# Optimization experiments

Measured on AMD Instinct MI355X. Metric: run time of the kernel, lower is better.

## Reference

```python
import jax, jax.numpy as jnp
import numpy as np

B = 128
NE = 14951   # num entities (FB15k)
NR = 1345    # num relations
D = 200      # complex embedding dim (real+imag concatenated)
NL = 116     # number of numerical literal relations


def setup_inputs() -> dict:
    key = jax.random.key(0)
    ks = jax.random.split(key, 8)
    e1_idx = jax.random.randint(ks[0], (B,), 0, NE)
    r_idx = jax.random.randint(ks[1], (B,), 0, NR)
    E = jax.random.normal(ks[2], (NE, D), dtype=jnp.float32) * 0.1
    R = jax.random.normal(ks[3], (NR, D), dtype=jnp.float32) * 0.1
    nf_weights = jax.random.normal(ks[4], (NR, NL), dtype=jnp.float32) * 0.1
    numerical_literals = jax.random.uniform(ks[5], (NE, NL), dtype=jnp.float32)
    c = jax.random.normal(ks[6], (NL,), dtype=jnp.float32) * 0.1
    var = jax.random.uniform(ks[7], (NL,), dtype=jnp.float32) * 0.5 + 0.1  # positive variances
    return {"e1_idx": e1_idx, "r_idx": r_idx, "E": E, "R": R,
            "nf_weights": nf_weights, "numerical_literals": numerical_literals,
            "c": c, "var": var}


def reference(e1_idx, r_idx, E, R, nf_weights, numerical_literals, c, var):
    d2 = E.shape[1] // 2
    e1 = E[e1_idx]            # [B, D]
    r = R[r_idx]              # [B, D]
    e1_real, e1_img = e1[:, :d2], e1[:, d2:]
    r_real, r_img = r[:, :d2], r[:, d2:]
    E_real, E_img = E[:, :d2], E[:, d2:]

    # ComplEx score against all entities: [B, NE]
    score_l = ((e1_real * r_real) @ E_real.T
               + (e1_real * r_img) @ E_img.T
               + (e1_img * r_real) @ E_img.T
               - (e1_img * r_img) @ E_real.T)

    # KBLN numerical-literal branch
    n_h = numerical_literals[e1_idx]                         # [B, NL]
    n = n_h[:, None, :] - numerical_literals[None, :, :]     # [B, NE, NL]
    phi = jnp.exp(-jnp.square(n - c) / var)                  # RBF, [B, NE, NL]
    w_nf = nf_weights[r_idx]                                 # [B, NL]
    score_n = jnp.einsum('ben,bn->be', phi, w_nf)            # [B, NE]

    return jax.nn.sigmoid(score_l + score_n)
```

## Files before the change

### kernel.cpp

```cpp
#include <hip/hip_runtime.h>

#define B     128
#define NE    14951
#define NEP   14976
#define NR    1345
#define D     200
#define NL    116
#define D2    100
#define EB    4
#define LOG2E 1.4426950408889634f

#define OFF_ET8  0
#define OFF_LT4  (OFF_ET8 + 25*NEP*4)
#define OFF_WB   (OFF_LT4 + 29*NEP*2)
#define OFF_UB   (OFF_WB + 128*200)
#define OFF_FB   (OFF_UB + 128*116)
#define OFF_NQ   (OFF_FB + 128*116)
#define WS_FLOATS (OFF_NQ + 128)
#define WS_NEEDED ((size_t)WS_FLOATS * 4)

__device__ __forceinline__ unsigned bf16rne(float f) {
    unsigned u = __float_as_uint(f);
    u += 0x7FFFu + ((u >> 16) & 1u);
    return u >> 16;
}
#define BF2F_LO(u) __uint_as_float((u) << 16)
#define BF2F_HI(u) __uint_as_float((u) & 0xffff0000u)

#define NB_A 1638
#define NB_B 1872
#define NB_C 64

__global__ __launch_bounds__(256) void prep_all(
    const int* __restrict__ e1_idx, const int* __restrict__ r_idx,
    const float* __restrict__ E, const float* __restrict__ R,
    const float* __restrict__ nf, const float* __restrict__ lit,
    const float* __restrict__ c, const float* __restrict__ var,
    float* __restrict__ ws)
{
    const int bid = blockIdx.x;
    const int t   = threadIdx.x;

    if (bid < NB_A) {
        const int ebk = bid % 234;
        const int cq  = (bid / 234) * 4 + (t >> 6);
        const int e   = ebk * 64 + (t & 63);
        if (cq >= 25) return;
        uint4 o = make_uint4(0u, 0u, 0u, 0u);
        if (e < NE) {
            float4 a = *(const float4*)(E + e*D + 8*cq);
            float4 b = *(const float4*)(E + e*D + 8*cq + 4);
            o.x = bf16rne(a.x) | (bf16rne(a.y) << 16);
            o.y = bf16rne(a.z) | (bf16rne(a.w) << 16);
            o.z = bf16rne(b.x) | (bf16rne(b.y) << 16);
            o.w = bf16rne(b.z) | (bf16rne(b.w) << 16);
        }
        ((uint4*)(ws + OFF_ET8))[cq*NEP + e] = o;
    } else if (bid < NB_A + NB_B) {
        const int idx = bid - NB_A;
        const int ebk = idx % 234;
        const int cq  = (idx / 234) * 4 + (t >> 6);
        const int e   = ebk * 64 + (t & 63);
        if (cq >= 29) return;
        uint2 o = make_uint2(0u, 0u);
        if (e < NE) {
            float4 L = *(const float4*)(lit + e*NL + 4*cq);
            o.x = bf16rne(L.x) | (bf16rne(L.y) << 16);
            o.y = bf16rne(L.z) | (bf16rne(L.w) << 16);
        }
        ((uint2*)(ws + OFF_LT4))[cq*NEP + e] = o;
    } else {
        const int b  = (bid - NB_A - NB_B) * 2 + (t >> 7);
        const int tt = t & 127;
        const int e1 = e1_idx[b];
        const int r  = r_idx[b];
        float* wb = ws + OFF_WB;
        float* ub = ws + OFF_UB;
        float* fb = ws + OFF_FB;
        if (tt < D2) {
            float e1r = E[e1*D + tt],      e1i = E[e1*D + D2 + tt];
            float rr  = R[r*D + tt],       ri  = R[r*D + D2 + tt];
            wb[b*D + tt]      = e1r*rr - e1i*ri;
            wb[b*D + D2 + tt] = e1r*ri + e1i*rr;
        }
        if (tt < NL) {
            float a = lit[e1*NL + tt] - c[tt];
            float q = -LOG2E / var[tt];
            ub[b*NL + tt] = -2.0f * q * a;
            fb[b*NL + tt] = nf[r*NL + tt] * __builtin_amdgcn_exp2f(q * a * a);
            if (b == 0) ws[OFF_NQ + tt] = q;
        }
    }
}


#define SL_STEP(pf, cq) do {                                              \
    float e0f = BF2F_LO((pf).x), e1f = BF2F_HI((pf).x);                   \
    float e2f = BF2F_LO((pf).y), e3f = BF2F_HI((pf).y);                   \
    float e4f = BF2F_LO((pf).z), e5f = BF2F_HI((pf).z);                   \
    float e6f = BF2F_LO((pf).w), e7f = BF2F_HI((pf).w);                   \
    _Pragma("unroll")                                                     \
    for (int j = 0; j < EB; ++j) {                                        \
        float4 wa = *(const float4*)(wb + (b0+j)*D + 8*(cq));             \
        float4 wc = *(const float4*)(wb + (b0+j)*D + 8*(cq) + 4);         \
        acc[j] = fmaf(wa.x, e0f, acc[j]);                                 \
        acc[j] = fmaf(wa.y, e1f, acc[j]);                                 \
        acc[j] = fmaf(wa.z, e2f, acc[j]);                                 \
        acc[j] = fmaf(wa.w, e3f, acc[j]);                                 \
        acc[j] = fmaf(wc.x, e4f, acc[j]);                                 \
        acc[j] = fmaf(wc.y, e5f, acc[j]);                                 \
        acc[j] = fmaf(wc.z, e6f, acc[j]);                                 \
        acc[j] = fmaf(wc.w, e7f, acc[j]);                                 \
    }                                                                     \
} while (0)

#define SN_STEP(lv, cq) do {                                              \
    float L0 = BF2F_LO((lv).x), L1 = BF2F_HI((lv).x);                     \
    float L2 = BF2F_LO((lv).y), L3 = BF2F_HI((lv).y);                     \
    float4 q = *(const float4*)(nq + 4*(cq));                             \
    float s0 = (q.x*L0)*L0, s1 = (q.y*L1)*L1;                             \
    float s2 = (q.z*L2)*L2, s3 = (q.w*L3)*L3;                             \
    _Pragma("unroll")                                                     \
    for (int j = 0; j < EB; ++j) {                                        \
        float4 uj = *(const float4*)(ub + (b0+j)*NL + 4*(cq));            \
        float4 fj = *(const float4*)(fb + (b0+j)*NL + 4*(cq));            \
        acc[j] = fmaf(fj.x, __builtin_amdgcn_exp2f(fmaf(uj.x, L0, s0)), acc[j]); \
        acc[j] = fmaf(fj.y, __builtin_amdgcn_exp2f(fmaf(uj.y, L1, s1)), acc[j]); \
        acc[j] = fmaf(fj.z, __builtin_amdgcn_exp2f(fmaf(uj.z, L2, s2)), acc[j]); \
        acc[j] = fmaf(fj.w, __builtin_amdgcn_exp2f(fmaf(uj.w, L3, s3)), acc[j]); \
    }                                                                     \
} while (0)

__global__ __launch_bounds__(128) void score_kernel(
    const float* __restrict__ et8, const float* __restrict__ lt4,
    const float* __restrict__ wb,  const float* __restrict__ ub,
    const float* __restrict__ fb,  const float* __restrict__ nq,
    float* __restrict__ out)
{
    const int lid  = blockIdx.x;
    const int p    = (lid & 7) * 468 + (lid >> 3);
    const int eblk = p >> 5;
    const int bblk = p & 31;
    const int e    = eblk * 128 + threadIdx.x;
    const int b0   = bblk * EB;

    float acc[EB];
#pragma unroll
    for (int j = 0; j < EB; ++j) acc[j] = 0.f;

    const uint4* E4 = (const uint4*)et8;
    const uint2* L4 = (const uint2*)lt4;

    {
        uint4 pf0 = E4[0*NEP + e];
        uint4 pf1 = E4[1*NEP + e];
        uint4 pf2 = E4[2*NEP + e];
        uint4 pf3 = E4[3*NEP + e];
        for (int cq0 = 0; cq0 < 20; cq0 += 4) {
            SL_STEP(pf0, cq0 + 0); pf0 = E4[(cq0 + 4)*NEP + e];
            SL_STEP(pf1, cq0 + 1); pf1 = E4[(cq0 + 5)*NEP + e];
            SL_STEP(pf2, cq0 + 2); pf2 = E4[(cq0 + 6)*NEP + e];
            SL_STEP(pf3, cq0 + 3); pf3 = E4[(cq0 + 7)*NEP + e];
        }
        SL_STEP(pf0, 20); pf0 = E4[24*NEP + e];
        SL_STEP(pf1, 21);
        SL_STEP(pf2, 22);
        SL_STEP(pf3, 23);
        SL_STEP(pf0, 24);
    }

    {
        uint2 lv0 = L4[0*NEP + e];
        uint2 lv1 = L4[1*NEP + e];
        uint2 lv2 = L4[2*NEP + e];
        uint2 lv3 = L4[3*NEP + e];
        for (int cq0 = 0; cq0 < 24; cq0 += 4) {
            SN_STEP(lv0, cq0 + 0); lv0 = L4[(cq0 + 4)*NEP + e];
            SN_STEP(lv1, cq0 + 1); lv1 = L4[(cq0 + 5)*NEP + e];
            SN_STEP(lv2, cq0 + 2); lv2 = L4[(cq0 + 6)*NEP + e];
            SN_STEP(lv3, cq0 + 3); lv3 = L4[(cq0 + 7)*NEP + e];
        }
        SN_STEP(lv0, 24); lv0 = L4[28*NEP + e];
        SN_STEP(lv1, 25);
        SN_STEP(lv2, 26);
        SN_STEP(lv3, 27);
        SN_STEP(lv0, 28);
    }

    if (e < NE) {
#pragma unroll
        for (int j = 0; j < EB; ++j) {
            float s = __builtin_amdgcn_rcpf(1.0f + __builtin_amdgcn_exp2f(acc[j] * -LOG2E));
            out[(b0+j)*NE + e] = s;
        }
    }
}


#define ET  4
#define OFF_W   0
#define OFF_A   25600
#define OFF_WNF 40448
#define OFF_NQL 55296

__global__ __launch_bounds__(128) void prep_kernel_legacy(
    const int* __restrict__ e1_idx, const int* __restrict__ r_idx,
    const float* __restrict__ E, const float* __restrict__ R,
    const float* __restrict__ nf, const float* __restrict__ lit,
    const float* __restrict__ c, const float* __restrict__ var,
    float* __restrict__ ws)
{
    const int b = blockIdx.x;
    const int t = threadIdx.x;
    const int e1 = e1_idx[b];
    const int r  = r_idx[b];
    if (t < D2) {
        float e1r = E[e1*D + t], e1i = E[e1*D + D2 + t];
        float rr  = R[r*D + t],  ri  = R[r*D + D2 + t];
        ws[OFF_W + (t >> 2)*512        + (b << 2) + (t & 3)] = e1r*rr - e1i*ri;
        ws[OFF_W + ((t >> 2) + 25)*512 + (b << 2) + (t & 3)] = e1r*ri + e1i*rr;
    }
    if (t < NL) {
        ws[OFF_A   + (t >> 2)*512 + (b << 2) + (t & 3)] = lit[e1*NL + t] - c[t];
        ws[OFF_WNF + (t >> 2)*512 + (b << 2) + (t & 3)] = nf[r*NL + t];
        if (b == 0) ws[OFF_NQL + t] = -LOG2E / var[t];
    }
}

__global__ __launch_bounds__(128) void main_kernel_legacy(
    const float* __restrict__ E, const float* __restrict__ lit,
    const float* __restrict__ ws, float* __restrict__ out)
{
    const int b  = threadIdx.x;
    const int e0 = blockIdx.x * ET;
    const float4* w4   = (const float4*)(ws + OFF_W);
    const float4* a4   = (const float4*)(ws + OFF_A);
    const float4* wnf4 = (const float4*)(ws + OFF_WNF);
    const float*  nqv  = ws + OFF_NQL;
    int eidx[ET];
#pragma unroll
    for (int j = 0; j < ET; ++j) eidx[j] = min(e0 + j, NE - 1);
    float acc[ET];
#pragma unroll
    for (int j = 0; j < ET; ++j) acc[j] = 0.0f;
    for (int dc = 0; dc < D; dc += 4) {
        float4 wv = w4[(dc >> 2)*B + b];
#pragma unroll
        for (int j = 0; j < ET; ++j) {
            float4 ev = *(const float4*)(E + eidx[j]*D + dc);
            acc[j] = fmaf(wv.x, ev.x, acc[j]);
            acc[j] = fmaf(wv.y, ev.y, acc[j]);
            acc[j] = fmaf(wv.z, ev.z, acc[j]);
            acc[j] = fmaf(wv.w, ev.w, acc[j]);
        }
    }
    for (int lc = 0; lc < NL; lc += 4) {
        float4 av = a4[(lc >> 2)*B + b];
        float4 wv = wnf4[(lc >> 2)*B + b];
        float4 q  = *(const float4*)(nqv + lc);
#pragma unroll
        for (int j = 0; j < ET; ++j) {
            float4 lv = *(const float4*)(lit + eidx[j]*NL + lc);
            float t0 = av.x - lv.x, t1 = av.y - lv.y, t2 = av.z - lv.z, t3 = av.w - lv.w;
            acc[j] += wv.x * __builtin_amdgcn_exp2f(t0*t0*q.x);
            acc[j] += wv.y * __builtin_amdgcn_exp2f(t1*t1*q.y);
            acc[j] += wv.z * __builtin_amdgcn_exp2f(t2*t2*q.z);
            acc[j] += wv.w * __builtin_amdgcn_exp2f(t3*t3*q.w);
        }
    }
#pragma unroll
    for (int j = 0; j < ET; ++j) {
        float s = 1.0f / (1.0f + __builtin_amdgcn_exp2f(acc[j] * -LOG2E));
        int e = e0 + j;
        if (e < NE) out[b*NE + e] = s;
    }
}


extern "C" void kernel_launch(void* const* d_in, const int* in_sizes, int n_in,
                              void* d_out, int out_size, void* d_ws, size_t ws_size,
                              hipStream_t stream) {
    const int*   e1_idx = (const int*)d_in[0];
    const int*   r_idx  = (const int*)d_in[1];
    const float* E      = (const float*)d_in[2];
    const float* R      = (const float*)d_in[3];
    const float* nf     = (const float*)d_in[4];
    const float* lit    = (const float*)d_in[5];
    const float* c      = (const float*)d_in[6];
    const float* var    = (const float*)d_in[7];
    float* out = (float*)d_out;
    float* ws  = (float*)d_ws;

    if (ws_size >= WS_NEEDED) {
        prep_all<<<NB_A + NB_B + NB_C, 256, 0, stream>>>(
            e1_idx, r_idx, E, R, nf, lit, c, var, ws);
        score_kernel<<<117 * 32, 128, 0, stream>>>(
            ws + OFF_ET8, ws + OFF_LT4,
            ws + OFF_WB, ws + OFF_UB, ws + OFF_FB, ws + OFF_NQ, out);
    } else {
        prep_kernel_legacy<<<B, 128, 0, stream>>>(e1_idx, r_idx, E, R, nf, lit, c, var, ws);
        main_kernel_legacy<<<(NE + ET - 1)/ET, B, 0, stream>>>(E, lit, ws, out);
    }
}
```

Before: 63.90 us.

## Move ComplEx score to separate MFMA bf16 GEMM kernel, score kernel adds RBF

Splits the ComplEx bilinear score out of the fused scalar-FMA score kernel into a dedicated GEMM kernel using 16x16x32 bf16 MFMA instructions. The query weights are now also packed to bf16 in the prep kernel, and the entity tensor is padded to 28 chunks. The GEMM writes a 128 x NEP fp32 intermediate to the workspace, which the RBF score kernel reads back to seed its accumulators. This frees the score kernel from FMA work, at the cost of an extra launch, about 7.6 MB of intermediate traffic, and bf16 rounding of the query weights.

Result: faster. 53.53 us (-16.2%).

```diff
diff --git a/kernel.cpp b/kernel.cpp
--- a/kernel.cpp
+++ b/kernel.cpp
@@ -10,10 +10,14 @@
 #define EB    4
 #define LOG2E 1.4426950408889634f
 
-#define OFF_ET8  0
-#define OFF_LT4  (OFF_ET8 + 25*NEP*4)
-#define OFF_WB   (OFF_LT4 + 29*NEP*2)
-#define OFF_UB   (OFF_WB + 128*200)
+typedef __attribute__((ext_vector_type(8))) short bf16x8;
+typedef __attribute__((ext_vector_type(4))) float f32x4;
+
+#define OFF_ET   0
+#define OFF_WA   (OFF_ET + 28*NEP*4)
+#define OFF_LT   (OFF_WA + 28*128*4)
+#define OFF_SL   (OFF_LT + 29*NEP*2)
+#define OFF_UB   (OFF_SL + 128*NEP)
 #define OFF_FB   (OFF_UB + 128*116)
 #define OFF_NQ   (OFF_FB + 128*116)
 #define WS_FLOATS (OFF_NQ + 128)
@@ -38,6 +42,7 @@
     const float* __restrict__ c, const float* __restrict__ var,
     float* __restrict__ ws)
 {
+    __shared__ float lwb[2][224];
     const int bid = blockIdx.x;
     const int t   = threadIdx.x;
 
@@ -45,9 +50,8 @@
         const int ebk = bid % 234;
         const int cq  = (bid / 234) * 4 + (t >> 6);
         const int e   = ebk * 64 + (t & 63);
-        if (cq >= 25) return;
         uint4 o = make_uint4(0u, 0u, 0u, 0u);
-        if (e < NE) {
+        if (e < NE && cq < 25) {
             float4 a = *(const float4*)(E + e*D + 8*cq);
             float4 b = *(const float4*)(E + e*D + 8*cq + 4);
             o.x = bf16rne(a.x) | (bf16rne(a.y) << 16);
@@ -55,7 +59,7 @@
             o.z = bf16rne(b.x) | (bf16rne(b.y) << 16);
             o.w = bf16rne(b.z) | (bf16rne(b.w) << 16);
         }
-        ((uint4*)(ws + OFF_ET8))[cq*NEP + e] = o;
+        ((uint4*)(ws + OFF_ET))[cq*NEP + e] = o;
     } else if (bid < NB_A + NB_B) {
         const int idx = bid - NB_A;
         const int ebk = idx % 234;
@@ -68,51 +72,68 @@
             o.x = bf16rne(L.x) | (bf16rne(L.y) << 16);
             o.y = bf16rne(L.z) | (bf16rne(L.w) << 16);
         }
-        ((uint2*)(ws + OFF_LT4))[cq*NEP + e] = o;
+        ((uint2*)(ws + OFF_LT))[cq*NEP + e] = o;
     } else {
-        const int b  = (bid - NB_A - NB_B) * 2 + (t >> 7);
-        const int tt = t & 127;
+        const int cb  = bid - NB_A - NB_B;
+        const int sub = t >> 7;
+        const int b   = cb*2 + sub;
+        const int tt  = t & 127;
         const int e1 = e1_idx[b];
         const int r  = r_idx[b];
-        float* wb = ws + OFF_WB;
-        float* ub = ws + OFF_UB;
-        float* fb = ws + OFF_FB;
         if (tt < D2) {
             float e1r = E[e1*D + tt],      e1i = E[e1*D + D2 + tt];
             float rr  = R[r*D + tt],       ri  = R[r*D + D2 + tt];
-            wb[b*D + tt]      = e1r*rr - e1i*ri;
-            wb[b*D + D2 + tt] = e1r*ri + e1i*rr;
-        }
+            lwb[sub][tt]      = e1r*rr - e1i*ri;
+            lwb[sub][D2 + tt] = e1r*ri + e1i*rr;
+        }
+        if (tt >= 100 && tt < 124) lwb[sub][100 + tt] = 0.f;
         if (tt < NL) {
             float a = lit[e1*NL + tt] - c[tt];
             float q = -LOG2E / var[tt];
-            ub[b*NL + tt] = -2.0f * q * a;
-            fb[b*NL + tt] = nf[r*NL + tt] * __builtin_amdgcn_exp2f(q * a * a);
-            if (b == 0) ws[OFF_NQ + tt] = q;
-        }
-    }
-}
-
-
-#define SL_STEP(pf, cq) do {                                              \
-    float e0f = BF2F_LO((pf).x), e1f = BF2F_HI((pf).x);                   \
-    float e2f = BF2F_LO((pf).y), e3f = BF2F_HI((pf).y);                   \
-    float e4f = BF2F_LO((pf).z), e5f = BF2F_HI((pf).z);                   \
-    float e6f = BF2F_LO((pf).w), e7f = BF2F_HI((pf).w);                   \
-    _Pragma("unroll")                                                     \
-    for (int j = 0; j < EB; ++j) {                                        \
-        float4 wa = *(const float4*)(wb + (b0+j)*D + 8*(cq));             \
-        float4 wc = *(const float4*)(wb + (b0+j)*D + 8*(cq) + 4);         \
-        acc[j] = fmaf(wa.x, e0f, acc[j]);                                 \
-        acc[j] = fmaf(wa.y, e1f, acc[j]);                                 \
-        acc[j] = fmaf(wa.z, e2f, acc[j]);                                 \
-        acc[j] = fmaf(wa.w, e3f, acc[j]);                                 \
-        acc[j] = fmaf(wc.x, e4f, acc[j]);                                 \
-        acc[j] = fmaf(wc.y, e5f, acc[j]);                                 \
-        acc[j] = fmaf(wc.z, e6f, acc[j]);                                 \
-        acc[j] = fmaf(wc.w, e7f, acc[j]);                                 \
-    }                                                                     \
-} while (0)
+            (ws + OFF_UB)[b*NL + tt] = -2.0f * q * a;
+            (ws + OFF_FB)[b*NL + tt] = nf[r*NL + tt] * __builtin_amdgcn_exp2f(q * a * a);
+            if (b == 0) (ws + OFF_NQ)[tt] = q;
+        }
+        __syncthreads();
+        if (tt < 28) {
+            const float* w8 = &lwb[sub][8*tt];
+            uint4 o;
+            o.x = bf16rne(w8[0]) | (bf16rne(w8[1]) << 16);
+            o.y = bf16rne(w8[2]) | (bf16rne(w8[3]) << 16);
+            o.z = bf16rne(w8[4]) | (bf16rne(w8[5]) << 16);
+            o.w = bf16rne(w8[6]) | (bf16rne(w8[7]) << 16);
+            ((uint4*)(ws + OFF_WA))[tt*128 + b] = o;
+        }
+    }
+}
+
+
+__global__ __launch_bounds__(256) void gemm_kernel(
+    const uint4* __restrict__ et, const uint4* __restrict__ wa,
+    float* __restrict__ sl)
+{
+    const int gw = blockIdx.x * 4 + (threadIdx.x >> 6);
+    const int l  = threadIdx.x & 63;
+    const int mb = gw / 936;
+    const int nb = gw - mb*936;
+    const int lane16 = l & 15;
+    const int grp    = l >> 4;
+    const int e = nb*16 + lane16;
+
+    f32x4 acc = {0.f, 0.f, 0.f, 0.f};
+#pragma unroll
+    for (int kc = 0; kc < 7; ++kc) {
+        const int s = kc*4 + grp;
+        bf16x8 a = *(const bf16x8*)(wa + s*128 + mb*16 + lane16);
+        bf16x8 b = *(const bf16x8*)(et + s*NEP + e);
+        acc = __builtin_amdgcn_mfma_f32_16x16x32_bf16(a, b, acc, 0, 0, 0);
+    }
+    const int brow = mb*16 + grp*4;
+#pragma unroll
+    for (int r = 0; r < 4; ++r)
+        sl[(brow + r)*NEP + e] = acc[r];
+}
+
 
 #define SN_STEP(lv, cq) do {                                              \
     float L0 = BF2F_LO((lv).x), L1 = BF2F_HI((lv).x);                     \
@@ -132,10 +153,9 @@
 } while (0)
 
 __global__ __launch_bounds__(128) void score_kernel(
-    const float* __restrict__ et8, const float* __restrict__ lt4,
-    const float* __restrict__ wb,  const float* __restrict__ ub,
-    const float* __restrict__ fb,  const float* __restrict__ nq,
-    float* __restrict__ out)
+    const float* __restrict__ lt4, const float* __restrict__ sl,
+    const float* __restrict__ ub,  const float* __restrict__ fb,
+    const float* __restrict__ nq,  float* __restrict__ out)
 {
     const int lid  = blockIdx.x;
     const int p    = (lid & 7) * 468 + (lid >> 3);
@@ -146,28 +166,9 @@
 
     float acc[EB];
 #pragma unroll
-    for (int j = 0; j < EB; ++j) acc[j] = 0.f;
-
-    const uint4* E4 = (const uint4*)et8;
+    for (int j = 0; j < EB; ++j) acc[j] = sl[(b0+j)*NEP + e];
+
     const uint2* L4 = (const uint2*)lt4;
-
-    {
-        uint4 pf0 = E4[0*NEP + e];
-        uint4 pf1 = E4[1*NEP + e];
-        uint4 pf2 = E4[2*NEP + e];
-        uint4 pf3 = E4[3*NEP + e];
-        for (int cq0 = 0; cq0 < 20; cq0 += 4) {
-            SL_STEP(pf0, cq0 + 0); pf0 = E4[(cq0 + 4)*NEP + e];
-            SL_STEP(pf1, cq0 + 1); pf1 = E4[(cq0 + 5)*NEP + e];
-            SL_STEP(pf2, cq0 + 2); pf2 = E4[(cq0 + 6)*NEP + e];
-            SL_STEP(pf3, cq0 + 3); pf3 = E4[(cq0 + 7)*NEP + e];
-        }
-        SL_STEP(pf0, 20); pf0 = E4[24*NEP + e];
-        SL_STEP(pf1, 21);
-        SL_STEP(pf2, 22);
-        SL_STEP(pf3, 23);
-        SL_STEP(pf0, 24);
-    }
 
     {
         uint2 lv0 = L4[0*NEP + e];
@@ -294,9 +295,10 @@
     if (ws_size >= WS_NEEDED) {
         prep_all<<<NB_A + NB_B + NB_C, 256, 0, stream>>>(
             e1_idx, r_idx, E, R, nf, lit, c, var, ws);
+        gemm_kernel<<<1872, 256, 0, stream>>>(
+            (const uint4*)(ws + OFF_ET), (const uint4*)(ws + OFF_WA), ws + OFF_SL);
         score_kernel<<<117 * 32, 128, 0, stream>>>(
-            ws + OFF_ET8, ws + OFF_LT4,
-            ws + OFF_WB, ws + OFF_UB, ws + OFF_FB, ws + OFF_NQ, out);
+            ws + OFF_LT, ws + OFF_SL, ws + OFF_UB, ws + OFF_FB, ws + OFF_NQ, out);
     } else {
         prep_kernel_legacy<<<B, 128, 0, stream>>>(e1_idx, r_idx, E, R, nf, lit, c, var, ws);
         main_kernel_legacy<<<(NE + ET - 1)/ET, B, 0, stream>>>(E, lit, ws, out);
```
